# Kernel optimization log

Hardware: AMD Instinct MI355X
Metric: run time of the kernel (lower is better)

## Reference

```python
import jax, jax.numpy as jnp
import numpy as np
import math

LMAX = 2            # input lmax
LMAX_OUT = 2 * LMAX # gaunt product output lmax
RES_BETA = 20
RES_ALPHA = 39
N = 2048
MUL = 64
C = 64
BRANCHES = [(1, 1), (1, -1), (-1, 1)]  # (p_val1, p_val2) per branch


def _real_sh_grid(lmax, res_beta, res_alpha):
    """Real orthonormal spherical harmonics on a Gauss-Legendre x uniform-alpha grid.
    Returns Y [(lmax+1)^2, res_beta, res_alpha] and quadrature weights qw [res_beta]
    (beta GL weight times 2*pi/res_alpha alpha weight)."""
    x, w = np.polynomial.legendre.leggauss(res_beta)  # x = cos(beta)
    phi = np.linspace(0.0, 2.0 * np.pi, res_alpha, endpoint=False)
    # associated Legendre P[l, m] on x via standard recurrences
    P = np.zeros((lmax + 1, lmax + 1, res_beta))
    P[0, 0] = 1.0
    s = np.sqrt(1.0 - x ** 2)
    for m in range(1, lmax + 1):
        P[m, m] = -(2 * m - 1) * s * P[m - 1, m - 1]
    for m in range(lmax):
        P[m + 1, m] = (2 * m + 1) * x * P[m, m]
    for m in range(lmax + 1):
        for l in range(m + 2, lmax + 1):
            P[l, m] = ((2 * l - 1) * x * P[l - 1, m] - (l + m - 1) * P[l - 2, m]) / (l - m)
    Y = np.zeros(((lmax + 1) ** 2, res_beta, res_alpha))
    idx = 0
    for l in range(lmax + 1):
        for m in range(-l, l + 1):
            am = abs(m)
            K = math.sqrt((2 * l + 1) / (4 * math.pi) * math.factorial(l - am) / math.factorial(l + am))
            if m == 0:
                ang = np.ones(res_alpha)
            elif m > 0:
                ang = math.sqrt(2.0) * np.cos(m * phi)
            else:
                ang = math.sqrt(2.0) * np.sin(am * phi)
            Y[idx] = K * P[l, am][:, None] * ang[None, :]
            idx += 1
    qw = w * (2.0 * np.pi / res_alpha)
    return Y.astype(np.float32), qw.astype(np.float32)


def setup_inputs() -> dict:
    key = jax.random.key(0)
    k1, k2, k3, k4, k5 = jax.random.split(key, 5)
    # inputs carry both parities per l: [N, mul, parity(2), (lmax+1)^2]
    x1 = jax.random.normal(k1, (N, MUL, 2, (LMAX + 1) ** 2), dtype=jnp.float32)
    x2 = jax.random.normal(k2, (N, MUL, 2, (LMAX + 1) ** 2), dtype=jnp.float32)
    # per-branch, per-l linear weights (e3nn Linear mixes multiplicities within each irrep)
    W1 = jax.random.normal(k3, (3, LMAX + 1, MUL, C), dtype=jnp.float32)
    W2 = jax.random.normal(k4, (3, LMAX + 1, MUL, C), dtype=jnp.float32)
    Wout = jax.random.normal(k5, (3, LMAX_OUT + 1, C, C), dtype=jnp.float32)
    Yfull, qw = _real_sh_grid(LMAX_OUT, RES_BETA, RES_ALPHA)
    Y_in = jnp.asarray(Yfull[: (LMAX + 1) ** 2])   # [9, B, A]
    Y_out = jnp.asarray(Yfull)                     # [25, B, A]
    return {"x1": x1, "x2": x2, "W1": W1, "W2": W2, "Wout": Wout,
            "Y_in": Y_in, "Y_out": Y_out, "qw": jnp.asarray(qw)}


def _project(x, W, p_val):
    """e3nn Linear to s2_irreps(LMAX, p_val)*C: for each l, take the input block with
    parity p_val*(-1)^l and mix multiplicities. x [N,mul,2,L2], W [L, mul, C] -> [N, C, L2]."""
    blocks = []
    inv_sqrt_mul = 1.0 / np.sqrt(x.shape[1])
    for l in range(LMAX + 1):
        pidx = 0 if p_val * ((-1) ** l) == 1 else 1  # 0 = even, 1 = odd parity slot
        sl = slice(l * l, (l + 1) * (l + 1))
        blocks.append(jnp.einsum('nmk,mc->nck', x[:, :, pidx, sl], W[l]) * inv_sqrt_mul)
    return jnp.concatenate(blocks, axis=-1)  # [N, C, (LMAX+1)^2]


def _gaunt_branch(x1, x2, W1b, W2b, Woutb, p1, p2, Y_in, Y_out, qw):
    c1 = _project(x1, W1b, p1)                      # [N, C, 9]
    c2 = _project(x2, W2b, p2)
    # SH -> grid (inverse spherical transform)
    s1 = jnp.einsum('ncl,lba->ncba', c1, Y_in)      # [N, C, B, A]
    s2 = jnp.einsum('ncl,lba->ncba', c2, Y_in)
    # pointwise multiply on S2, then grid -> SH (forward transform w/ quadrature)
    co = jnp.einsum('ncba,lba,b->ncl', s1 * s2, Y_out, qw)  # [N, C, 25]
    # linear_out: per-l [C -> C] mixing
    inv_sqrt_c = 1.0 / np.sqrt(co.shape[1])
    outs = []
    for l in range(LMAX_OUT + 1):
        sl = slice(l * l, (l + 1) * (l + 1))
        outs.append(jnp.einsum('nck,cd->ndk', co[:, :, sl], Woutb[l]) * inv_sqrt_c)
    return jnp.concatenate(outs, axis=-1)           # [N, C, 25]


def reference(x1, x2, W1, W2, Wout, Y_in, Y_out, qw):
    outs = [_gaunt_branch(x1, x2, W1[b], W2[b], Wout[b], p1, p2, Y_in, Y_out, qw)
            for b, (p1, p2) in enumerate(BRANCHES)]
    return jnp.stack(outs, axis=1)                  # [N, 3, C, 25] (concat over parities)
```

## Files before the change

### kernel.cpp

```cpp
#include <hip/hip_runtime.h>
#include <utility>


#define NN 2048

__host__ __device__ constexpr int l_of9(int i)  { return i < 1 ? 0 : (i < 4 ? 1 : 2); }
__host__ __device__ constexpr int l_of25(int k) { return k < 1 ? 0 : (k < 4 ? 1 : (k < 9 ? 2 : (k < 16 ? 3 : 4))); }
__host__ __device__ constexpr int iabs_(int v)  { return v < 0 ? -v : v; }

__host__ __device__ constexpr bool gmask(int k, int i, int j) {
    const int l3 = l_of25(k), m3 = k - l3 * l3 - l3;
    const int l1 = l_of9(i),  m1 = i - l1 * l1 - l1;
    const int l2 = l_of9(j),  m2 = j - l2 * l2 - l2;
    if (((l1 + l2 + l3) & 1) != 0) return false;
    if (l3 > l1 + l2 || l3 < iabs_(l1 - l2)) return false;
    const int am3 = iabs_(m3);
    return (am3 == iabs_(m1 + m2)) || (am3 == iabs_(m1 - m2));
}

struct GTab {
    int po[82];
    int pc[81];
    int kl[81][12];
    constexpr GTab() : po{}, pc{}, kl{} {
        int off = 0;
        for (int ij = 0; ij < 81; ++ij) {
            po[ij] = off;
            const int i = ij / 9, j = ij % 9;
            int cnum = 0;
            for (int k = 0; k < 25; ++k)
                if (gmask(k, i, j)) kl[ij][cnum++] = k;
            pc[ij] = cnum;
            off += (cnum + 3) & ~3;
        }
        po[81] = off;
    }
};
constexpr GTab GT{};

__global__ __launch_bounds__(256) void gaunt_pack_kernel(
    const float* __restrict__ Y_in, const float* __restrict__ Y_out,
    const float* __restrict__ qw, float* __restrict__ gp)
{
    const int ij = blockIdx.x;
    const int i = ij / 9, j = ij % 9;
    const int t = threadIdx.x;

    __shared__ float yy[780];
    __shared__ float ps[25][8];
    __shared__ float gr[25];

    for (int p = t; p < 780; p += 256)
        yy[p] = Y_in[i * 780 + p] * Y_in[j * 780 + p] * qw[p / 39];
    __syncthreads();

    if (t < 200) {
        const int k = t >> 3, s = t & 7;
        const float* yo = Y_out + k * 780;
        const int p1 = (s * 98 + 98 < 780) ? (s * 98 + 98) : 780;
        float a = 0.f;
        for (int p = s * 98; p < p1; ++p) a = fmaf(yy[p], yo[p], a);
        ps[k][s] = a;
    }
    __syncthreads();

    if (t < 25) {
        float a = 0.f;
#pragma unroll
        for (int s = 0; s < 8; ++s) a += ps[t][s];
        gr[t] = a;
    }
    __syncthreads();

    const int cntp = (GT.pc[ij] + 3) & ~3;
    if (t < cntp)
        gp[GT.po[ij] + t] = (t < GT.pc[ij]) ? gr[GT.kl[ij][t]] : 0.f;
}

template <int IJ, int... Ts>
__device__ __forceinline__ void gaunt_apply(const float (&g)[12], float pij,
    float (&cov)[25], std::integer_sequence<int, Ts...>)
{
    ((cov[GT.kl[IJ][Ts]] = fmaf(g[Ts], pij, cov[GT.kl[IJ][Ts]])), ...);
}

template <int IJ>
__device__ __forceinline__ void gaunt_pair(const float* __restrict__ gp,
    const float (&c1)[9], const float (&c2)[9], float (&cov)[25])
{
    constexpr int cnt = GT.pc[IJ];
    if constexpr (cnt > 0) {
        constexpr int base = GT.po[IJ];
        constexpr int nv = (cnt + 3) / 4;
        const float pij = c1[IJ / 9] * c2[IJ % 9];
        float g[12];
#pragma unroll
        for (int q = 0; q < nv; ++q) {
            const float4 v = ((const float4*)(gp + base))[q];
            g[4 * q] = v.x; g[4 * q + 1] = v.y; g[4 * q + 2] = v.z; g[4 * q + 3] = v.w;
        }
        gaunt_apply<IJ>(g, pij, cov, std::make_integer_sequence<int, cnt>{});
    }
}

template <int I, int... Js>
__device__ __forceinline__ void gaunt_row(const float* __restrict__ gp,
    const float (&c1)[9], const float (&c2)[9], float (&cov)[25],
    std::integer_sequence<int, Js...>)
{
    (gaunt_pair<I * 9 + Js>(gp, c1, c2, cov), ...);
    __builtin_amdgcn_sched_barrier(0);
}

template <int... Is>
__device__ __forceinline__ void gaunt_all(const float* __restrict__ gp,
    const float (&c1)[9], const float (&c2)[9], float (&cov)[25],
    std::integer_sequence<int, Is...>)
{
    (gaunt_row<Is>(gp, c1, c2, cov, std::make_integer_sequence<int, 9>{}), ...);
}

template <int E1, int E2>
__device__ __forceinline__ void fused_body(
    const float* __restrict__ x1, const float* __restrict__ x2,
    const float* __restrict__ W1, const float* __restrict__ W2,
    const float* __restrict__ Wout, const float* __restrict__ gp,
    float* __restrict__ out, float* __restrict__ cs, int b)
{
    const int t = threadIdx.x;
    const int c = t & 63;
    const int w = __builtin_amdgcn_readfirstlane(t >> 6);
    const int n = blockIdx.x * 4 + w;

    const float* x1n = x1 + (size_t)n * 1152;
    const float* x2n = x2 + (size_t)n * 1152;
    const float* W1b = W1 + (size_t)b * 3 * 4096 + c;
    const float* W2b = W2 + (size_t)b * 3 * 4096 + c;

    float a1[9] = {0,0,0,0,0,0,0,0,0};
    float a2[9] = {0,0,0,0,0,0,0,0,0};

#pragma unroll 1
    for (int mp = 0; mp < 32; ++mp) {
        const float4* p1 = (const float4*)(x1n + mp * 36);
        const float4* p2 = (const float4*)(x2n + mp * 36);
        float xs1[36], xs2[36];
#pragma unroll
        for (int q = 0; q < 9; ++q) {
            const float4 t1 = p1[q], t2 = p2[q];
            xs1[4*q] = t1.x; xs1[4*q+1] = t1.y; xs1[4*q+2] = t1.z; xs1[4*q+3] = t1.w;
            xs2[4*q] = t2.x; xs2[4*q+1] = t2.y; xs2[4*q+2] = t2.z; xs2[4*q+3] = t2.w;
        }
        float w1v[3][2], w2v[3][2];
#pragma unroll
        for (int l = 0; l < 3; ++l)
#pragma unroll
            for (int mi = 0; mi < 2; ++mi) {
                const int moff = (l * 64 + mp * 2 + mi) * 64;
                w1v[l][mi] = W1b[moff];
                w2v[l][mi] = W2b[moff];
            }
#pragma unroll
        for (int l = 0; l < 3; ++l) {
            const int O1 = ((l & 1) ^ E1) * 9 + l * l;
            const int O2 = ((l & 1) ^ E2) * 9 + l * l;
#pragma unroll
            for (int mi = 0; mi < 2; ++mi)
#pragma unroll
                for (int ii = 0; ii <= 2 * l; ++ii) {
                    a1[l*l+ii] = fmaf(xs1[O1 + 18*mi + ii], w1v[l][mi], a1[l*l+ii]);
                    a2[l*l+ii] = fmaf(xs2[O2 + 18*mi + ii], w2v[l][mi], a2[l*l+ii]);
                }
        }
    }

    float c1[9], c2[9];
#pragma unroll
    for (int i = 0; i < 9; ++i) { c1[i] = a1[i] * 0.125f; c2[i] = a2[i] * 0.125f; }

    float cov[25] = {0,0,0,0,0,0,0,0,0,0,0,0,0,0,0,0,0,0,0,0,0,0,0,0,0};
    gaunt_all(gp, c1, c2, cov, std::make_integer_sequence<int, 9>{});

    float* csw = cs + w * (64 * 28);
#pragma unroll
    for (int kk = 0; kk < 25; ++kk) csw[c * 28 + kk] = cov[kk];

    const float* WoB = Wout + (size_t)b * 5 * 4096 + c;
    float acc[25];
#pragma unroll
    for (int kk = 0; kk < 25; ++kk) acc[kk] = 0.f;

#pragma unroll 1
    for (int d = 0; d < 64; ++d) {
        float row[28];
#pragma unroll
        for (int q = 0; q < 7; ++q) {
            const float4 v = *(const float4*)&csw[d * 28 + 4 * q];
            row[4*q] = v.x; row[4*q+1] = v.y; row[4*q+2] = v.z; row[4*q+3] = v.w;
        }
        float wv[5];
#pragma unroll
        for (int l3 = 0; l3 < 5; ++l3) wv[l3] = WoB[(l3 * 64 + d) * 64];
#pragma unroll
        for (int k = 0; k < 25; ++k)
            acc[k] = fmaf(row[k], wv[l_of25(k)], acc[k]);
    }

    float* op = out + (((size_t)n * 3 + b) * 64 + c) * 25;
#pragma unroll
    for (int k = 0; k < 25; ++k) op[k] = acc[k] * 0.125f;
}

__global__ __launch_bounds__(256, 5) void fused_kernel(
    const float* __restrict__ x1, const float* __restrict__ x2,
    const float* __restrict__ W1, const float* __restrict__ W2,
    const float* __restrict__ Wout, const float* __restrict__ gp,
    float* __restrict__ out)
{
    __shared__ __align__(16) float cs[4 * 64 * 28];
    const int b = blockIdx.y;
    if (b == 0)      fused_body<0, 0>(x1, x2, W1, W2, Wout, gp, out, cs, 0);
    else if (b == 1) fused_body<0, 1>(x1, x2, W1, W2, Wout, gp, out, cs, 1);
    else             fused_body<1, 0>(x1, x2, W1, W2, Wout, gp, out, cs, 2);
}

extern "C" void kernel_launch(void* const* d_in, const int* in_sizes, int n_in,
                              void* d_out, int out_size, void* d_ws, size_t ws_size,
                              hipStream_t stream) {
    const float* x1    = (const float*)d_in[0];
    const float* x2    = (const float*)d_in[1];
    const float* W1    = (const float*)d_in[2];
    const float* W2    = (const float*)d_in[3];
    const float* Wout  = (const float*)d_in[4];
    const float* Y_in  = (const float*)d_in[5];
    const float* Y_out = (const float*)d_in[6];
    const float* qw    = (const float*)d_in[7];
    float* outp = (float*)d_out;
    float* gp   = (float*)d_ws;

    gaunt_pack_kernel<<<81, 256, 0, stream>>>(Y_in, Y_out, qw, gp);
    fused_kernel<<<dim3(NN / 4, 3), 256, 0, stream>>>(x1, x2, W1, W2, Wout, gp, outp);
}
```

Measured before the change: 141.6 us.

## Split output channel mixing into separate kernel using output buffer as staging

Moves the per-l Wout channel mixing out of the fused projection/Gaunt kernel into a new mix_kernel. The fused kernel now writes the Gaunt coefficients transposed ([k][c]) into the output buffer. The mix kernel reads them back per (n, branch), applies Wout and rewrites the result in place through shared memory. This frees the shared-memory staging and registers from the fused kernel, which now requests higher occupancy. The cost is an extra kernel launch and a full global round trip of the intermediate tensor.

Result: no change. 140.2 us (-1.0%).

```diff
diff --git a/kernel.cpp b/kernel.cpp
--- a/kernel.cpp
+++ b/kernel.cpp
@@ -124,8 +124,7 @@
 __device__ __forceinline__ void fused_body(
     const float* __restrict__ x1, const float* __restrict__ x2,
     const float* __restrict__ W1, const float* __restrict__ W2,
-    const float* __restrict__ Wout, const float* __restrict__ gp,
-    float* __restrict__ out, float* __restrict__ cs, int b)
+    const float* __restrict__ gp, float* __restrict__ out, int b)
 {
     const int t = threadIdx.x;
     const int c = t & 63;
@@ -181,47 +180,78 @@
     float cov[25] = {0,0,0,0,0,0,0,0,0,0,0,0,0,0,0,0,0,0,0,0,0,0,0,0,0};
     gaunt_all(gp, c1, c2, cov, std::make_integer_sequence<int, 9>{});
 
-    float* csw = cs + w * (64 * 28);
-#pragma unroll
-    for (int kk = 0; kk < 25; ++kk) csw[c * 28 + kk] = cov[kk];
-
-    const float* WoB = Wout + (size_t)b * 5 * 4096 + c;
-    float acc[25];
-#pragma unroll
-    for (int kk = 0; kk < 25; ++kk) acc[kk] = 0.f;
-
-#pragma unroll 1
-    for (int d = 0; d < 64; ++d) {
-        float row[28];
-#pragma unroll
-        for (int q = 0; q < 7; ++q) {
-            const float4 v = *(const float4*)&csw[d * 28 + 4 * q];
-            row[4*q] = v.x; row[4*q+1] = v.y; row[4*q+2] = v.z; row[4*q+3] = v.w;
-        }
-        float wv[5];
-#pragma unroll
-        for (int l3 = 0; l3 < 5; ++l3) wv[l3] = WoB[(l3 * 64 + d) * 64];
-#pragma unroll
-        for (int k = 0; k < 25; ++k)
-            acc[k] = fmaf(row[k], wv[l_of25(k)], acc[k]);
-    }
-
-    float* op = out + (((size_t)n * 3 + b) * 64 + c) * 25;
-#pragma unroll
-    for (int k = 0; k < 25; ++k) op[k] = acc[k] * 0.125f;
-}
-
-__global__ __launch_bounds__(256, 5) void fused_kernel(
+    float* cob = out + ((size_t)n * 3 + b) * 1600 + c;
+#pragma unroll
+    for (int k = 0; k < 25; ++k) cob[k * 64] = cov[k];
+}
+
+__global__ __launch_bounds__(256, 6) void fused_kernel(
     const float* __restrict__ x1, const float* __restrict__ x2,
     const float* __restrict__ W1, const float* __restrict__ W2,
-    const float* __restrict__ Wout, const float* __restrict__ gp,
-    float* __restrict__ out)
-{
-    __shared__ __align__(16) float cs[4 * 64 * 28];
+    const float* __restrict__ gp, float* __restrict__ out)
+{
     const int b = blockIdx.y;
-    if (b == 0)      fused_body<0, 0>(x1, x2, W1, W2, Wout, gp, out, cs, 0);
-    else if (b == 1) fused_body<0, 1>(x1, x2, W1, W2, Wout, gp, out, cs, 1);
-    else             fused_body<1, 0>(x1, x2, W1, W2, Wout, gp, out, cs, 2);
+    if (b == 0)      fused_body<0, 0>(x1, x2, W1, W2, gp, out, 0);
+    else if (b == 1) fused_body<0, 1>(x1, x2, W1, W2, gp, out, 1);
+    else             fused_body<1, 0>(x1, x2, W1, W2, gp, out, 2);
+}
+
+__global__ __launch_bounds__(64, 6) void mix_kernel(
+    const float* __restrict__ Wout, float* __restrict__ io)
+{
+    const int n = blockIdx.x;
+    const int b = blockIdx.y;
+    const int c = threadIdx.x;
+
+    __shared__ float st[1600];
+
+    const float* cob = io + ((size_t)n * 3 + b) * 1600;
+    const float* WoB = Wout + (size_t)b * 5 * 4096 + c;
+
+    float acc[25];
+#pragma unroll
+    for (int k = 0; k < 25; ++k) acc[k] = 0.f;
+
+#pragma unroll 1
+    for (int dc = 0; dc < 16; ++dc) {
+        const int d0 = dc * 4;
+        float wr[5][4];
+#pragma unroll
+        for (int l3 = 0; l3 < 5; ++l3)
+#pragma unroll
+            for (int q = 0; q < 4; ++q)
+                wr[l3][q] = WoB[(size_t)(l3 * 64 + d0 + q) * 64];
+
+#pragma unroll
+        for (int kg = 0; kg < 5; ++kg) {
+#pragma unroll
+            for (int kk = 0; kk < 5; ++kk) {
+                const int k = kg * 5 + kk;
+                const int l3 = l_of25(k);
+                const float4 cv = *(const float4*)(cob + k * 64 + d0);
+                acc[k] = fmaf(cv.x, wr[l3][0], acc[k]);
+                acc[k] = fmaf(cv.y, wr[l3][1], acc[k]);
+                acc[k] = fmaf(cv.z, wr[l3][2], acc[k]);
+                acc[k] = fmaf(cv.w, wr[l3][3], acc[k]);
+            }
+            __builtin_amdgcn_sched_barrier(0);
+        }
+    }
+
+#pragma unroll
+    for (int k = 0; k < 25; ++k) st[c * 25 + k] = acc[k] * 0.125f;
+    __syncthreads();
+
+    float* op = io + ((size_t)n * 3 + b) * 1600;
+#pragma unroll
+    for (int r = 0; r < 6; ++r) {
+        const float4 v = *(const float4*)&st[(r * 64 + c) * 4];
+        *(float4*)(op + (r * 64 + c) * 4) = v;
+    }
+    if (c < 16) {
+        const float4 v = *(const float4*)&st[(384 + c) * 4];
+        *(float4*)(op + (384 + c) * 4) = v;
+    }
 }
 
 extern "C" void kernel_launch(void* const* d_in, const int* in_sizes, int n_in,
@@ -239,5 +269,6 @@
     float* gp   = (float*)d_ws;
 
     gaunt_pack_kernel<<<81, 256, 0, stream>>>(Y_in, Y_out, qw, gp);
-    fused_kernel<<<dim3(NN / 4, 3), 256, 0, stream>>>(x1, x2, W1, W2, Wout, gp, outp);
-}
+    fused_kernel<<<dim3(NN / 4, 3), 256, 0, stream>>>(x1, x2, W1, W2, gp, outp);
+    mix_kernel<<<dim3(NN, 3), 64, 0, stream>>>(Wout, outp);
+}
```

## Stage x inputs through LDS with async global_load_lds double buffering and coalesce output

Applied to the files above, without the earlier changes.

The projection loop now stages x1/x2 chunks into shared memory with global_load_lds in double-buffered form, instead of having each lane issue redundant direct float4 global loads. The grid is transposed so the three branches for the same node group run in adjacent blocks, which should improve cache reuse of x. The 1/64 scale is folded into the packed gaunt coefficients, and the output is transposed through LDS so it can be written with coalesced float4 stores. Occupancy hint drops from 5 to 4, and extra __syncthreads are added per chunk.

Result: slower. 173.8 us (+22.7%).

```diff
diff --git a/kernel.cpp b/kernel.cpp
--- a/kernel.cpp
+++ b/kernel.cpp
@@ -74,7 +74,7 @@
 
     const int cntp = (GT.pc[ij] + 3) & ~3;
     if (t < cntp)
-        gp[GT.po[ij] + t] = (t < GT.pc[ij]) ? gr[GT.kl[ij][t]] : 0.f;
+        gp[GT.po[ij] + t] = (t < GT.pc[ij]) ? gr[GT.kl[ij][t]] * 0.015625f : 0.f;
 }
 
 template <int IJ, int... Ts>
@@ -120,108 +120,161 @@
     (gaunt_row<Is>(gp, c1, c2, cov, std::make_integer_sequence<int, 9>{}), ...);
 }
 
+typedef __attribute__((address_space(1))) const unsigned int gas_u32;
+typedef __attribute__((address_space(3))) unsigned int las_u32;
+__device__ __forceinline__ void gll16(const void* g, void* l) {
+    __builtin_amdgcn_global_load_lds((gas_u32*)g, (las_u32*)l, 16, 0, 0);
+}
+
 template <int E1, int E2>
-__device__ __forceinline__ void fused_body(
+__device__ __forceinline__ void k1_body(
     const float* __restrict__ x1, const float* __restrict__ x2,
     const float* __restrict__ W1, const float* __restrict__ W2,
     const float* __restrict__ Wout, const float* __restrict__ gp,
-    float* __restrict__ out, float* __restrict__ cs, int b)
-{
-    const int t = threadIdx.x;
-    const int c = t & 63;
-    const int w = __builtin_amdgcn_readfirstlane(t >> 6);
-    const int n = blockIdx.x * 4 + w;
-
-    const float* x1n = x1 + (size_t)n * 1152;
-    const float* x2n = x2 + (size_t)n * 1152;
-    const float* W1b = W1 + (size_t)b * 3 * 4096 + c;
-    const float* W2b = W2 + (size_t)b * 3 * 4096 + c;
+    float* __restrict__ out, float* smemf, int b)
+{
+    const int t  = threadIdx.x;
+    const int c  = t & 63;
+    const int w  = t >> 6;
+    const int n0 = blockIdx.y * 4;
+    const int n  = n0 + w;
+
+    char* smem = (char*)smemf;
+
+    auto stage = [&](int mc, int buf) {
+        {
+            const int g   = t;
+            const int arr = g / 144;
+            const int gg  = g - arr * 144;
+            const int n_l = gg / 36;
+            const int r4  = (gg - n_l * 36) * 4;
+            const float* src = (arr ? x2 : x1) +
+                (size_t)(n0 + n_l) * 1152 + mc * 144 + r4;
+            char* dst = smem + buf * 4608 + (t & ~63) * 16;
+            gll16(src, dst);
+        }
+        if (t < 32) {
+            const int gg  = 256 + t - 144;
+            const int r4  = (gg - 108) * 4;
+            const float* src = x2 + (size_t)(n0 + 3) * 1152 + mc * 144 + r4;
+            char* dst = smem + buf * 4608 + 4096;
+            gll16(src, dst);
+        }
+    };
+
+    const float* W1b = W1 + (size_t)b * 12288 + c;
+    const float* W2b = W2 + (size_t)b * 12288 + c;
 
     float a1[9] = {0,0,0,0,0,0,0,0,0};
     float a2[9] = {0,0,0,0,0,0,0,0,0};
 
+    stage(0, 0);
+    __syncthreads();
+
 #pragma unroll 1
-    for (int mp = 0; mp < 32; ++mp) {
-        const float4* p1 = (const float4*)(x1n + mp * 36);
-        const float4* p2 = (const float4*)(x2n + mp * 36);
-        float xs1[36], xs2[36];
-#pragma unroll
-        for (int q = 0; q < 9; ++q) {
-            const float4 t1 = p1[q], t2 = p2[q];
-            xs1[4*q] = t1.x; xs1[4*q+1] = t1.y; xs1[4*q+2] = t1.z; xs1[4*q+3] = t1.w;
-            xs2[4*q] = t2.x; xs2[4*q+1] = t2.y; xs2[4*q+2] = t2.z; xs2[4*q+3] = t2.w;
-        }
-        float w1v[3][2], w2v[3][2];
-#pragma unroll
-        for (int l = 0; l < 3; ++l)
-#pragma unroll
-            for (int mi = 0; mi < 2; ++mi) {
-                const int moff = (l * 64 + mp * 2 + mi) * 64;
-                w1v[l][mi] = W1b[moff];
-                w2v[l][mi] = W2b[moff];
+    for (int mc = 0; mc < 8; ++mc) {
+        const int buf = mc & 1;
+        if (mc < 7) stage(mc + 1, buf ^ 1);
+
+        const float* xb1 = smemf + buf * 1152 + w * 144;
+        const float* xb2 = smemf + buf * 1152 + 576 + w * 144;
+
+#pragma unroll 1
+        for (int mh = 0; mh < 2; ++mh) {
+            float w1r[3][4], w2r[3][4];
+#pragma unroll
+            for (int l = 0; l < 3; ++l)
+#pragma unroll
+                for (int mm = 0; mm < 4; ++mm) {
+                    const int o = (l * 64 + mc * 8 + mh * 4 + mm) * 64;
+                    w1r[l][mm] = W1b[o];
+                    w2r[l][mm] = W2b[o];
+                }
+#pragma unroll
+            for (int mm = 0; mm < 4; ++mm) {
+                const float* r1 = xb1 + (mh * 4 + mm) * 18;
+                const float* r2 = xb2 + (mh * 4 + mm) * 18;
+                float xv1[18], xv2[18];
+#pragma unroll
+                for (int q = 0; q < 9; ++q) {
+                    const float2 v1 = *(const float2*)(r1 + q * 2);
+                    const float2 v2 = *(const float2*)(r2 + q * 2);
+                    xv1[2*q] = v1.x; xv1[2*q+1] = v1.y;
+                    xv2[2*q] = v2.x; xv2[2*q+1] = v2.y;
+                }
+#pragma unroll
+                for (int l = 0; l < 3; ++l) {
+                    const int O1 = ((l & 1) ^ E1) * 9 + l * l;
+                    const int O2 = ((l & 1) ^ E2) * 9 + l * l;
+#pragma unroll
+                    for (int ii = 0; ii <= 2 * l; ++ii) {
+                        a1[l*l+ii] = fmaf(xv1[O1 + ii], w1r[l][mm], a1[l*l+ii]);
+                        a2[l*l+ii] = fmaf(xv2[O2 + ii], w2r[l][mm], a2[l*l+ii]);
+                    }
+                }
             }
-#pragma unroll
-        for (int l = 0; l < 3; ++l) {
-            const int O1 = ((l & 1) ^ E1) * 9 + l * l;
-            const int O2 = ((l & 1) ^ E2) * 9 + l * l;
-#pragma unroll
-            for (int mi = 0; mi < 2; ++mi)
-#pragma unroll
-                for (int ii = 0; ii <= 2 * l; ++ii) {
-                    a1[l*l+ii] = fmaf(xs1[O1 + 18*mi + ii], w1v[l][mi], a1[l*l+ii]);
-                    a2[l*l+ii] = fmaf(xs2[O2 + 18*mi + ii], w2v[l][mi], a2[l*l+ii]);
-                }
-        }
-    }
-
-    float c1[9], c2[9];
-#pragma unroll
-    for (int i = 0; i < 9; ++i) { c1[i] = a1[i] * 0.125f; c2[i] = a2[i] * 0.125f; }
+        }
+        __syncthreads();
+    }
 
     float cov[25] = {0,0,0,0,0,0,0,0,0,0,0,0,0,0,0,0,0,0,0,0,0,0,0,0,0};
-    gaunt_all(gp, c1, c2, cov, std::make_integer_sequence<int, 9>{});
-
-    float* csw = cs + w * (64 * 28);
-#pragma unroll
-    for (int kk = 0; kk < 25; ++kk) csw[c * 28 + kk] = cov[kk];
-
-    const float* WoB = Wout + (size_t)b * 5 * 4096 + c;
+    gaunt_all(gp, a1, a2, cov, std::make_integer_sequence<int, 9>{});
+
+    float* colw = smemf + w * 1792;
+#pragma unroll
+    for (int k = 0; k < 25; ++k) colw[c * 28 + k] = cov[k];
+
+    const float* WoB = Wout + (size_t)b * 20480 + c;
     float acc[25];
 #pragma unroll
-    for (int kk = 0; kk < 25; ++kk) acc[kk] = 0.f;
+    for (int k = 0; k < 25; ++k) acc[k] = 0.f;
 
 #pragma unroll 1
-    for (int d = 0; d < 64; ++d) {
-        float row[28];
-#pragma unroll
-        for (int q = 0; q < 7; ++q) {
-            const float4 v = *(const float4*)&csw[d * 28 + 4 * q];
-            row[4*q] = v.x; row[4*q+1] = v.y; row[4*q+2] = v.z; row[4*q+3] = v.w;
-        }
-        float wv[5];
-#pragma unroll
-        for (int l3 = 0; l3 < 5; ++l3) wv[l3] = WoB[(l3 * 64 + d) * 64];
-#pragma unroll
-        for (int k = 0; k < 25; ++k)
-            acc[k] = fmaf(row[k], wv[l_of25(k)], acc[k]);
-    }
-
-    float* op = out + (((size_t)n * 3 + b) * 64 + c) * 25;
-#pragma unroll
-    for (int k = 0; k < 25; ++k) op[k] = acc[k] * 0.125f;
-}
-
-__global__ __launch_bounds__(256, 5) void fused_kernel(
+    for (int dc = 0; dc < 16; ++dc) {
+        float wv[5][4];
+#pragma unroll
+        for (int l3 = 0; l3 < 5; ++l3)
+#pragma unroll
+            for (int dd = 0; dd < 4; ++dd)
+                wv[l3][dd] = WoB[(l3 * 64 + dc * 4 + dd) * 64];
+#pragma unroll
+        for (int dd = 0; dd < 4; ++dd) {
+            const float* row = colw + (dc * 4 + dd) * 28;
+            float f[28];
+#pragma unroll
+            for (int q = 0; q < 7; ++q) {
+                const float4 v = *(const float4*)(row + q * 4);
+                f[4*q] = v.x; f[4*q+1] = v.y; f[4*q+2] = v.z; f[4*q+3] = v.w;
+            }
+#pragma unroll
+            for (int k = 0; k < 25; ++k)
+                acc[k] = fmaf(f[k], wv[l_of25(k)][dd], acc[k]);
+        }
+    }
+
+#pragma unroll
+    for (int k = 0; k < 25; ++k) colw[c * 25 + k] = acc[k] * 0.125f;
+
+    float* on = out + ((size_t)n * 3 + b) * 1600;
+#pragma unroll
+    for (int r = 0; r < 6; ++r) {
+        const float4 v = *(const float4*)&colw[r * 256 + c * 4];
+        *(float4*)&on[r * 256 + c * 4] = v;
+    }
+    on[1536 + c] = colw[1536 + c];
+}
+
+__global__ __launch_bounds__(256, 4) void fused_kernel(
     const float* __restrict__ x1, const float* __restrict__ x2,
     const float* __restrict__ W1, const float* __restrict__ W2,
     const float* __restrict__ Wout, const float* __restrict__ gp,
     float* __restrict__ out)
 {
-    __shared__ __align__(16) float cs[4 * 64 * 28];
-    const int b = blockIdx.y;
-    if (b == 0)      fused_body<0, 0>(x1, x2, W1, W2, Wout, gp, out, cs, 0);
-    else if (b == 1) fused_body<0, 1>(x1, x2, W1, W2, Wout, gp, out, cs, 1);
-    else             fused_body<1, 0>(x1, x2, W1, W2, Wout, gp, out, cs, 2);
+    __shared__ __align__(16) float smemf[7168];
+    const int b = blockIdx.x;
+    if (b == 0)      k1_body<0, 0>(x1, x2, W1, W2, Wout, gp, out, smemf, 0);
+    else if (b == 1) k1_body<0, 1>(x1, x2, W1, W2, Wout, gp, out, smemf, 1);
+    else             k1_body<1, 0>(x1, x2, W1, W2, Wout, gp, out, smemf, 2);
 }
 
 extern "C" void kernel_launch(void* const* d_in, const int* in_sizes, int n_in,
@@ -239,5 +292,5 @@
     float* gp   = (float*)d_ws;
 
     gaunt_pack_kernel<<<81, 256, 0, stream>>>(Y_in, Y_out, qw, gp);
-    fused_kernel<<<dim3(NN / 4, 3), 256, 0, stream>>>(x1, x2, W1, W2, Wout, gp, outp);
-}
+    fused_kernel<<<dim3(3, NN / 4), 256, 0, stream>>>(x1, x2, W1, W2, Wout, gp, outp);
+}
```
